# Kernel optimization log

Hardware: AMD Instinct MI355X
Metric: run time of the kernel (lower is better)

## Reference

```python
import jax, jax.numpy as jnp
import numpy as np

B, NC, H, W, C = 4, 3, 112, 112, 128
HEADS, WS, SS = 4, 7, 3
HD = C // HEADS
SCALE = HD ** -0.5
NWIN = (H // WS) * (W // WS)
N = WS * WS  # tokens per window per contrast


def _rel_pos_index():
    # standard Swin relative position index over a WSxWS window
    c = np.stack(np.meshgrid(np.arange(WS), np.arange(WS), indexing='ij')).reshape(2, -1)
    r = (c[:, :, None] - c[:, None, :]).transpose(1, 2, 0)
    r[:, :, 0] += WS - 1
    r[:, :, 1] += WS - 1
    r[:, :, 0] *= 2 * WS - 1
    return r.sum(-1)  # (N, N) int

RPI = _rel_pos_index()


def _attn_mask():
    # SW-MSA mask built exactly as in __init__ (shift active since 0 < SS < WS)
    img = np.zeros((H, W))
    sl = (slice(0, -WS), slice(-WS, -SS), slice(-SS, None))
    cnt = 0
    for hh in sl:
        for ww in sl:
            img[hh, ww] = cnt
            cnt += 1
    mw = img.reshape(H // WS, WS, W // WS, WS).transpose(0, 2, 1, 3).reshape(-1, N)
    am = mw[:, None, :] - mw[:, :, None]  # unsqueeze(1) - unsqueeze(2)
    return jnp.asarray(np.where(am != 0, -100.0, 0.0), dtype=np.float32)  # (nW, N, N)

MASK = _attn_mask()


def win_part(x):
    # (B, n, H, W, C) -> (B*nW, n, WS, WS, C)
    b, n = x.shape[0], x.shape[1]
    x = x.reshape(b, n, H // WS, WS, W // WS, WS, C)
    return x.transpose(0, 2, 4, 1, 3, 5, 6).reshape(-1, n, WS, WS, C)


def win_rev(x, b):
    # (B*nW, n, WS, WS, C) -> (B, n, H, W, C)
    n = x.shape[1]
    x = x.reshape(b, H // WS, W // WS, n, WS, WS, C)
    return x.transpose(0, 3, 1, 4, 2, 5, 6).reshape(b, n, H, W, C)


def ln(x, g, bta):
    m = x.mean(-1, keepdims=True)
    v = ((x - m) ** 2).mean(-1, keepdims=True)
    return (x - m) * jax.lax.rsqrt(v + 1e-5) * g + bta


def win_attn(xq, xk, xv, wq, bq, wk, bk, wv, bv, wp, bp, rpb):
    B_, nq = xq.shape[0], xq.shape[1]
    nkv = xk.shape[1]
    Nq, Nkv = nq * N, nkv * N
    q = (xq.reshape(B_, Nq, C) @ wq + bq).reshape(B_, Nq, HEADS, HD).transpose(0, 2, 1, 3) * SCALE
    k = (xk.reshape(B_, Nkv, C) @ wk + bk).reshape(B_, Nkv, HEADS, HD).transpose(0, 2, 1, 3)
    v = (xv.reshape(B_, Nkv, C) @ wv + bv).reshape(B_, Nkv, HEADS, HD).transpose(0, 2, 1, 3)
    attn = jnp.einsum('bhqd,bhkd->bhqk', q, k)
    bias = jnp.tile(rpb[RPI].transpose(2, 0, 1), (1, nq, nkv))  # (HEADS, Nq, Nkv)
    attn = attn + bias[None]
    m = jnp.tile(MASK, (1, nq, nkv))  # (nW, Nq, Nkv)
    attn = attn.reshape(B_ // NWIN, NWIN, HEADS, Nq, Nkv) + m[None, :, None]
    attn = jax.nn.softmax(attn.reshape(B_, HEADS, Nq, Nkv), axis=-1)
    out = jnp.einsum('bhqk,bhkd->bhqd', attn, v).transpose(0, 2, 1, 3).reshape(B_, Nq, C) @ wp + bp
    return out.reshape(B_, nq, WS, WS, C)


def reference(x, x_kv, contrast_token, contrast_embed,
              n1g, n1b, n2g, n2b, n3g, n3b,
              sa_wq, sa_bq, sa_wk, sa_bk, sa_wv, sa_bv, sa_wp, sa_bp, sa_rpb,
              ca_wq, ca_bq, ca_wk, ca_bk, ca_wv, ca_bv, ca_wp, ca_bp, ca_rpb,
              m_w1, m_b1, m_w2, m_b2):
    ct = contrast_token[None, :, None, None, :]
    ce = contrast_embed[None, :, None, None, :]
    # --- shifted-window self-attention ---
    shortcut = x
    h = ln(x, n1g, n1b)
    h = jnp.roll(h, (-SS, -SS), axis=(2, 3))
    xw = win_part(h)
    xwe = xw + ct
    aw = win_attn(xwe, xwe, xw, sa_wq, sa_bq, sa_wk, sa_bk, sa_wv, sa_bv, sa_wp, sa_bp, sa_rpb)
    h = win_rev(aw, B)
    h = jnp.roll(h, (SS, SS), axis=(2, 3))
    x = shortcut + h
    # --- shifted-window cross-attention against x_kv ---
    shortcut = x
    h = ln(x, n2g, n2b)
    hs = jnp.roll(h, (-SS, -SS), axis=(2, 3))
    kvs = jnp.roll(x_kv, (-SS, -SS), axis=(2, 3))
    xw = win_part(hs)
    kw = win_part(kvs)
    aw = win_attn(xw + ct, kw + ce, kw, ca_wq, ca_bq, ca_wk, ca_bk, ca_wv, ca_bv, ca_wp, ca_bp, ca_rpb)
    h = win_rev(aw, B)
    h = jnp.roll(h, (SS, SS), axis=(2, 3))
    x = shortcut + h
    # --- MLP ---
    h = ln(x, n3g, n3b)
    h = jax.nn.gelu(h @ m_w1 + m_b1, approximate=False) @ m_w2 + m_b2
    return x + h


def setup_inputs():
    key = jax.random.key(0)
    ks = jax.random.split(key, 32)
    rn = lambda i, shp, s=1.0: jax.random.normal(ks[i], shp, dtype=jnp.float32) * s
    inp = {
        'x': rn(0, (B, NC, H, W, C)),
        'x_kv': rn(1, (B, NC, H, W, C)),
        'contrast_token': rn(2, (NC, C), 0.02),
        'contrast_embed': rn(3, (NC, C), 0.02),
        'n1g': jnp.ones((C,)), 'n1b': jnp.zeros((C,)),
        'n2g': jnp.ones((C,)), 'n2b': jnp.zeros((C,)),
        'n3g': jnp.ones((C,)), 'n3b': jnp.zeros((C,)),
    }
    i = 4
    for pre in ('sa', 'ca'):
        for nm in ('wq', 'wk', 'wv', 'wp'):
            inp[pre + '_' + nm] = rn(i, (C, C), 0.02)
            inp[pre + '_b' + nm[1]] = jnp.zeros((C,))
            i += 1
        inp[pre + '_rpb'] = rn(i, ((2 * WS - 1) ** 2, HEADS), 0.02)
        i += 1
    inp['m_w1'] = rn(i, (C, 4 * C), 0.02)
    inp['m_b1'] = jnp.zeros((4 * C,))
    inp['m_w2'] = rn(i + 1, (4 * C, C), 0.02)
    inp['m_b2'] = jnp.zeros((C,))
    return inp
```

## Files before the change

kernel.cpp:

```cpp
#include <hip/hip_runtime.h>
#include <hip/hip_bf16.h>

typedef __hip_bfloat16 bf16;

#define Bn    4
#define NCn   3
#define Hn    112
#define Wn    112
#define Cn    128
#define HEADS 4
#define WSn   7
#define SSn   3
#define HDn   32
#define WNt   1024
#define Tt    147
#define SCALE 0.17677669529663687f

#define SA    288
#define SH    1056
#define MT    48
#define MTOK  80

static const size_t NE = (size_t)Bn * NCn * Hn * Wn * Cn;

typedef float f32x4 __attribute__((ext_vector_type(4)));
typedef short s16x8 __attribute__((ext_vector_type(8)));
typedef short s16x4 __attribute__((ext_vector_type(4)));
#define MFMA(a,b,c) __builtin_amdgcn_mfma_f32_16x16x32_bf16((a),(b),(c),0,0,0)

#define P_QCSA 0
#define P_KCSA 384
#define P_QCCA 768
#define P_KCCA 1152
#define P_VCSA 1536
#define P_BPSA 1664
#define P_VCCA 1792
#define P_BPCA 1920
#define P_B1   2048
#define P_B2   2560
#define P_G1   2688
#define P_N1B  2816
#define P_G2   2944
#define P_N2B  3072
#define P_G3   3200
#define P_N3B  3328
#define P_RPBSA 3456
#define P_RPBCA 4132

#define W_SAQ 0
#define W_SAK 16384
#define W_SAV 32768
#define W_SAP 49152
#define W_CAQ 65536
#define W_CAK 81920
#define W_CAV 98304
#define W_CAP 114688
#define W_W1T 131072
#define W_W2T 196608

struct Ptrs { const void* p[32]; };

__device__ __forceinline__ float bf2f(bf16 v) { return __bfloat162float(v); }
__device__ __forceinline__ bf16  f2bf(float v) { return __float2bfloat16(v); }
__device__ __forceinline__ short f2bs(float v) { bf16 t = __float2bfloat16(v); return *reinterpret_cast<short*>(&t); }
__device__ __forceinline__ float bs2f(short v) { bf16 t = *reinterpret_cast<bf16*>(&v); return __bfloat162float(t); }

__device__ __forceinline__ float ldi(const void* __restrict__ p, size_t i, int f) {
    return f ? ((const float*)p)[i] : bf2f(((const bf16*)p)[i]);
}

__device__ __forceinline__ float gelu(float x) {
    float x2 = x * x;
    float arg = x * fmaf(x2, 0.0713548162f, 1.5957691216f);
    float e = __expf(arg);
    float r = __builtin_amdgcn_rcpf(1.f + e);
    return x - x * r;
}

__device__ __forceinline__ int tok_row(int wn, int t) {
    int b = wn >> 8, wrem = wn & 255, wi = wrem >> 4, wj = wrem & 15;
    int n = t / 49, p = t % 49, pi = p / 7, pj = p % 7;
    int i = (wi * 7 + pi + SSn) % Hn;
    int j = (wj * 7 + pj + SSn) % Wn;
    return ((b * NCn + n) * Hn + i) * Wn + j;
}

__global__ void k_detect(const unsigned int* __restrict__ xw, int* __restrict__ flag) {
    __shared__ int cnt;
    if (threadIdx.x == 0) cnt = 0;
    __syncthreads();
    int c = 0;
    for (int i = threadIdx.x; i < 8192; i += 256) {
        unsigned e = (xw[i] >> 7) & 0xffu;
        c += (e >= 100u && e <= 140u) ? 1 : 0;
    }
    atomicAdd(&cnt, c);
    __syncthreads();
    if (threadIdx.x == 0) *flag = (cnt < 4096) ? 1 : 0;
}

__global__ __launch_bounds__(256) void k_prep(Ptrs in, const int* __restrict__ dflag,
                                              float* __restrict__ P, bf16* __restrict__ wT,
                                              float* __restrict__ BMT) {
    const int f = *dflag;
    int b = blockIdx.x, tid = threadIdx.x;
    if (b == 0) {
        for (int t = tid; t < 384; t += 256) {
            int n = t >> 7, c = t & 127;
            float aq = 0.f, ak = 0.f, aq2 = 0.f, ak2 = 0.f;
            for (int d = 0; d < Cn; ++d) {
                float ctv = ldi(in.p[2], n * Cn + d, f);
                float cev = ldi(in.p[3], n * Cn + d, f);
                aq  += ctv * ldi(in.p[10], d * Cn + c, f);
                ak  += ctv * ldi(in.p[12], d * Cn + c, f);
                aq2 += ctv * ldi(in.p[19], d * Cn + c, f);
                ak2 += cev * ldi(in.p[21], d * Cn + c, f);
            }
            P[P_QCSA + t] = aq  + ldi(in.p[11], c, f);
            P[P_KCSA + t] = ak  + ldi(in.p[13], c, f);
            P[P_QCCA + t] = aq2 + ldi(in.p[20], c, f);
            P[P_KCCA + t] = ak2 + ldi(in.p[22], c, f);
        }
    } else if (b == 1) {
        if (tid < 128) {
            P[P_VCSA + tid] = ldi(in.p[15], tid, f);
            P[P_BPSA + tid] = ldi(in.p[17], tid, f);
            P[P_VCCA + tid] = ldi(in.p[24], tid, f);
            P[P_BPCA + tid] = ldi(in.p[26], tid, f);
            P[P_B2   + tid] = ldi(in.p[31], tid, f);
            P[P_G1   + tid] = ldi(in.p[4],  tid, f);
            P[P_N1B  + tid] = ldi(in.p[5],  tid, f);
            P[P_G2   + tid] = ldi(in.p[6],  tid, f);
            P[P_N2B  + tid] = ldi(in.p[7],  tid, f);
            P[P_G3   + tid] = ldi(in.p[8],  tid, f);
            P[P_N3B  + tid] = ldi(in.p[9],  tid, f);
        }
        for (int t = tid; t < 512; t += 256) P[P_B1 + t] = ldi(in.p[29], t, f);
    } else if (b < 66) {
        const int map[8] = {10, 12, 14, 16, 19, 21, 23, 25};
        int unit = (b - 2) * 4 + (tid >> 6), lane = tid & 63;
        int mat = unit >> 5, ntks = unit & 31;
        int ntile = ntks >> 2, ks = ntks & 3;
        int n = ntile * 16 + (lane & 15), k0 = ks * 32 + (lane >> 4) * 8;
        const void* src = in.p[map[mat]];
        s16x8 v;
        #pragma unroll
        for (int j = 0; j < 8; ++j) v[j] = f2bs(ldi(src, (size_t)(k0 + j) * 128 + n, f));
        *(s16x8*)(wT + mat * 16384 + ((size_t)ntks * 64 + lane) * 8) = v;
    } else if (b < 130) {
        int unit = (b - 66) * 4 + (tid >> 6), lane = tid & 63;
        s16x8 v;
        if (unit < 128) {
            int ntile = unit >> 2, ks = unit & 3;
            int n = ntile * 16 + (lane & 15), k0 = ks * 32 + (lane >> 4) * 8;
            #pragma unroll
            for (int j = 0; j < 8; ++j) v[j] = f2bs(ldi(in.p[28], (size_t)(k0 + j) * 512 + n, f));
            *(s16x8*)(wT + W_W1T + ((size_t)unit * 64 + lane) * 8) = v;
        } else {
            int b2 = unit - 128;
            int ntile = b2 >> 4, ks = b2 & 15;
            int n = ntile * 16 + (lane & 15), k0 = ks * 32 + (lane >> 4) * 8;
            #pragma unroll
            for (int j = 0; j < 8; ++j) v[j] = f2bs(ldi(in.p[30], (size_t)(k0 + j) * 128 + n, f));
            *(s16x8*)(wT + W_W2T + ((size_t)b2 * 64 + lane) * 8) = v;
        }
    } else {
        int u = b - 130;
        int stage = u >> 4, pat = (u >> 2) & 3, h = u & 3;
        const void* rpb = in.p[stage ? 27 : 18];
        float* dst = BMT + (size_t)u * 2560;
        int er = pat >> 1, ec = pat & 1;
        for (int i = tid; i < 2560; i += 256) {
            float v = 0.f;
            int qp = i / 52, kp = i - qp * 52;
            if (qp < 49 && kp < 49) {
                int qpi = qp / 7, qpj = qp - qpi * 7, kpi = kp / 7, kpj = kp - kpi * 7;
                float bias = ldi(rpb, ((qpi - kpi + 6) * 13 + (qpj - kpj + 6)) * HEADS + h, f);
                int rq = (er ? (qpi < 4 ? 1 : 2) : 0) * 3 + (ec ? (qpj < 4 ? 1 : 2) : 0);
                int rk = (er ? (kpi < 4 ? 1 : 2) : 0) * 3 + (ec ? (kpj < 4 ? 1 : 2) : 0);
                v = bias + (rq == rk ? 0.f : -100.f);
            }
            dst[i] = v;
        }
    }
}

__device__ __forceinline__ void ln_inplace(char* __restrict__ rp, const float* __restrict__ gb) {
    float s = 0.f, s2 = 0.f;
    #pragma unroll
    for (int c8 = 0; c8 < 16; ++c8) {
        s16x8 v = *(const s16x8*)(rp + c8 * 16);
        #pragma unroll
        for (int j = 0; j < 8; ++j) { float fv = bs2f(v[j]); s += fv; s2 += fv * fv; }
    }
    float mean = s * (1.f / 128.f);
    float rstd = rsqrtf(s2 * (1.f / 128.f) - mean * mean + 1e-5f);
    #pragma unroll
    for (int c8 = 0; c8 < 16; ++c8) {
        s16x8 v = *(const s16x8*)(rp + c8 * 16);
        #pragma unroll
        for (int j = 0; j < 8; ++j) {
            int col = c8 * 8 + j;
            v[j] = f2bs((bs2f(v[j]) - mean) * rstd * gb[col] + gb[128 + col]);
        }
        *(s16x8*)(rp + c8 * 16) = v;
    }
}

__global__ __launch_bounds__(256) void k_qkv_sa(
    const void* __restrict__ x, bf16* __restrict__ xr,
    const float* __restrict__ P, const bf16* __restrict__ wT,
    const int* __restrict__ dflag,
    bf16* __restrict__ tokQ, bf16* __restrict__ tokK, bf16* __restrict__ tokV) {
    const int f = *dflag;
    __shared__ char ldsA[MTOK * SA];
    __shared__ int rowIdx[MTOK];
    __shared__ float gb[256];
    int wn = blockIdx.x, halfb = blockIdx.y, tid = threadIdx.x;
    int t0 = halfb * MTOK;
    int nrows = halfb ? (Tt - MTOK) : MTOK;
    if (tid < nrows) rowIdx[tid] = tok_row(wn, t0 + tid);
    gb[tid] = tid < 128 ? P[P_G1 + tid] : P[P_N1B + tid - 128];
    if (halfb) for (int i = tid; i < 13 * SA / 4; i += 256) ((int*)(ldsA + 67 * SA))[i] = 0;
    __syncthreads();
    for (int idx = tid; idx < nrows * 16; idx += 256) {
        int t = idx >> 4, c8 = idx & 15;
        size_t g = (size_t)rowIdx[t] * Cn + c8 * 8;
        s16x8 v;
        if (f) {
            const float* s = (const float*)x + g;
            #pragma unroll
            for (int j = 0; j < 8; ++j) v[j] = f2bs(s[j]);
        } else {
            v = *(const s16x8*)((const bf16*)x + g);
        }
        *(s16x8*)(ldsA + t * SA + c8 * 16) = v;
        *(s16x8*)(xr + g) = v;
    }
    __syncthreads();
    if (tid < nrows) ln_inplace(ldsA + tid * SA, gb);
    __syncthreads();
    int wv = tid >> 6, lane = tid & 63, l15 = lane & 15, lg = lane >> 4;
    #pragma unroll 1
    for (int mat = 0; mat < 3; ++mat) {
        const bf16* W = wT + mat * 16384;
        bf16* dst = mat == 0 ? tokQ : (mat == 1 ? tokK : tokV);
        #pragma unroll 1
        for (int ni = 0; ni < 2; ++ni) {
            int nt = wv * 2 + ni;
            f32x4 acc[5] = {};
            #pragma unroll
            for (int ks = 0; ks < 4; ++ks) {
                s16x8 bfrag = *(const s16x8*)(W + (((nt << 2) + ks) * 64 + lane) * 8);
                #pragma unroll
                for (int mt = 0; mt < 5; ++mt) {
                    s16x8 af = *(const s16x8*)(ldsA + (mt * 16 + l15) * SA + ks * 64 + lg * 16);
                    acc[mt] = MFMA(bfrag, af, acc[mt]);
                }
            }
            int col0 = nt * 16 + lg * 4;
            #pragma unroll
            for (int mt = 0; mt < 5; ++mt) {
                int tl = mt * 16 + l15;
                if (tl < nrows) {
                    int t = t0 + tl;
                    int n = t / 49;
                    s16x4 pk;
                    if (mat == 0) {
                        f32x4 b4 = *(const f32x4*)(P + P_QCSA + n * 128 + col0);
                        #pragma unroll
                        for (int r = 0; r < 4; ++r) pk[r] = f2bs((acc[mt][r] + b4[r]) * SCALE);
                    } else if (mat == 1) {
                        f32x4 b4 = *(const f32x4*)(P + P_KCSA + n * 128 + col0);
                        #pragma unroll
                        for (int r = 0; r < 4; ++r) pk[r] = f2bs(acc[mt][r] + b4[r]);
                    } else {
                        f32x4 b4 = *(const f32x4*)(P + P_VCSA + col0);
                        #pragma unroll
                        for (int r = 0; r < 4; ++r) pk[r] = f2bs(acc[mt][r] + b4[r]);
                    }
                    *(s16x4*)(dst + ((size_t)wn * Tt + t) * Cn + col0) = pk;
                }
            }
        }
    }
}

__global__ __launch_bounds__(256) void k_attn(
    const bf16* __restrict__ Q, const bf16* __restrict__ K, const bf16* __restrict__ V,
    bf16* __restrict__ O, const float* __restrict__ BMbase) {
    __shared__ char ldsK[40 * 256];
    __shared__ char ldsV[32 * 336];
    __shared__ char ldsP[4 * 16 * 336];
    __shared__ float BM[2560];
    __shared__ float lArr[4][16];
    int wn = blockIdx.x, h = blockIdx.y, tid = threadIdx.x;
    int wi = (wn >> 4) & 15, wj = wn & 15;
    size_t base = (size_t)wn * Tt * Cn + h * HDn;
    for (int idx = tid; idx < 640; idx += 256) {
        int key = idx >> 2, ch = idx & 3;
        s16x8 kv = {}, vv = {};
        if (key < Tt) {
            kv = *(const s16x8*)(K + base + (size_t)key * Cn + ch * 8);
            vv = *(const s16x8*)(V + base + (size_t)key * Cn + ch * 8);
        }
        *(s16x8*)(ldsK + (key >> 2) * 256 + (key & 3) * 64 + ch * 16) = kv;
        #pragma unroll
        for (int j = 0; j < 8; ++j)
            *(short*)(ldsV + (ch * 8 + j) * 336 + key * 2) = vv[j];
    }
    {
        int pat = ((wi == 15) << 1) | (wj == 15);
        const f32x4* src = (const f32x4*)(BMbase + (size_t)(pat * 4 + h) * 2560);
        f32x4* dst4 = (f32x4*)BM;
        for (int i = tid; i < 640; i += 256) dst4[i] = src[i];
    }
    __syncthreads();
    int wv = tid >> 6, lane = tid & 63, l15 = lane & 15, lg = lane >> 4;
    char* myP = ldsP + wv * (16 * 336);
    int kpA[10];
    #pragma unroll
    for (int nt = 0; nt < 10; ++nt) {
        int key = nt * 16 + l15;
        kpA[nt] = key - (key >= 147 ? 147 : (key >= 98 ? 98 : (key >= 49 ? 49 : 0)));
    }
    for (int mt = wv; mt < 10; mt += 4) {
        int qrow = mt * 16 + l15; if (qrow > 146) qrow = 146;
        s16x8 qf = *(const s16x8*)(Q + base + (size_t)qrow * Cn + lg * 8);
        f32x4 acc[10];
        #pragma unroll
        for (int nt = 0; nt < 10; ++nt) {
            int key = nt * 16 + l15;
            s16x8 bfrag = *(const s16x8*)(ldsK + (key >> 2) * 256 + (key & 3) * 64 + lg * 16);
            f32x4 z = {};
            acc[nt] = MFMA(qf, bfrag, z);
        }
        float linv[4];
        #pragma unroll
        for (int r = 0; r < 4; ++r) {
            int row = mt * 16 + lg * 4 + r;
            int qp = row - (row >= 147 ? 147 : (row >= 98 ? 98 : (row >= 49 ? 49 : 0)));
            float s[10], m = -1e30f;
            #pragma unroll
            for (int nt = 0; nt < 10; ++nt) {
                float sv = acc[nt][r] + BM[qp * 52 + kpA[nt]];
                if (nt == 9 && l15 >= 3) sv = -1e30f;
                s[nt] = sv;
                m = fmaxf(m, sv);
            }
            #pragma unroll
            for (int off = 1; off < 16; off <<= 1) m = fmaxf(m, __shfl_xor(m, off));
            float l = 0.f;
            #pragma unroll
            for (int nt = 0; nt < 10; ++nt) {
                float p = (nt == 9 && l15 >= 3) ? 0.f : __expf(s[nt] - m);
                l += p;
                *(bf16*)(myP + (lg * 4 + r) * 336 + (nt * 16 + l15) * 2) = f2bf(p);
            }
            #pragma unroll
            for (int off = 1; off < 16; off <<= 1) l += __shfl_xor(l, off);
            linv[r] = 1.f / l;
        }
        if (l15 == 0) {
            #pragma unroll
            for (int r = 0; r < 4; ++r) lArr[wv][lg * 4 + r] = linv[r];
        }
        float myinv = lArr[wv][l15];
        #pragma unroll
        for (int ntv = 0; ntv < 2; ++ntv) {
            f32x4 ao = {};
            #pragma unroll
            for (int ks = 0; ks < 5; ++ks) {
                s16x8 af = *(const s16x8*)(myP + l15 * 336 + ks * 64 + lg * 16);
                s16x8 vf = *(const s16x8*)(ldsV + (ntv * 16 + l15) * 336 + ks * 64 + lg * 16);
                ao = MFMA(vf, af, ao);
            }
            int q = mt * 16 + l15;
            if (q < Tt) {
                s16x4 pk;
                #pragma unroll
                for (int r = 0; r < 4; ++r) pk[r] = f2bs(ao[r] * myinv);
                *(s16x4*)(O + base + (size_t)q * Cn + ntv * 16 + lg * 4) = pk;
            }
        }
    }
}

__global__ __launch_bounds__(256) void k_proj(
    const bf16* __restrict__ tokO, const float* __restrict__ P, const bf16* __restrict__ W,
    int bpOff, bf16* __restrict__ xr) {
    __shared__ char ldsA[MTOK * SA];
    __shared__ int rowIdx[MTOK];
    int wn = blockIdx.x, halfb = blockIdx.y, tid = threadIdx.x;
    int t0 = halfb * MTOK;
    int nrows = halfb ? (Tt - MTOK) : MTOK;
    if (tid < nrows) rowIdx[tid] = tok_row(wn, t0 + tid);
    if (halfb) for (int i = tid; i < 13 * SA / 4; i += 256) ((int*)(ldsA + 67 * SA))[i] = 0;
    __syncthreads();
    for (int idx = tid; idx < nrows * 16; idx += 256) {
        int t = idx >> 4, c8 = idx & 15;
        s16x8 v = *(const s16x8*)(tokO + ((size_t)wn * Tt + t0 + t) * Cn + c8 * 8);
        *(s16x8*)(ldsA + t * SA + c8 * 16) = v;
    }
    __syncthreads();
    int wv = tid >> 6, lane = tid & 63, l15 = lane & 15, lg = lane >> 4;
    #pragma unroll 1
    for (int ni = 0; ni < 2; ++ni) {
        int nt = wv * 2 + ni;
        f32x4 acc[5] = {};
        #pragma unroll
        for (int ks = 0; ks < 4; ++ks) {
            s16x8 bfrag = *(const s16x8*)(W + (((nt << 2) + ks) * 64 + lane) * 8);
            #pragma unroll
            for (int mt = 0; mt < 5; ++mt) {
                s16x8 af = *(const s16x8*)(ldsA + (mt * 16 + l15) * SA + ks * 64 + lg * 16);
                acc[mt] = MFMA(bfrag, af, acc[mt]);
            }
        }
        int col0 = nt * 16 + lg * 4;
        f32x4 bp4 = *(const f32x4*)(P + bpOff + col0);
        #pragma unroll
        for (int mt = 0; mt < 5; ++mt) {
            int tl = mt * 16 + l15;
            if (tl < nrows) {
                size_t o = (size_t)rowIdx[tl] * Cn + col0;
                s16x4 cur = *(const s16x4*)(xr + o);
                s16x4 pk;
                #pragma unroll
                for (int r = 0; r < 4; ++r) pk[r] = f2bs(bs2f(cur[r]) + acc[mt][r] + bp4[r]);
                *(s16x4*)(xr + o) = pk;
            }
        }
    }
}

__global__ __launch_bounds__(256) void k_proj_ca(
    const bf16* __restrict__ tokO, const float* __restrict__ P, const bf16* __restrict__ wT,
    const void* __restrict__ xkv, const int* __restrict__ dflag, bf16* __restrict__ xr,
    bf16* __restrict__ tokQ, bf16* __restrict__ tokK, bf16* __restrict__ tokV) {
    const int f = *dflag;
    __shared__ char ldsA[MTOK * SA];
    __shared__ int rowIdx[MTOK];
    __shared__ float gb[256];
    int wn = blockIdx.x, halfb = blockIdx.y, tid = threadIdx.x;
    int t0 = halfb * MTOK;
    int nrows = halfb ? (Tt - MTOK) : MTOK;
    if (tid < nrows) rowIdx[tid] = tok_row(wn, t0 + tid);
    gb[tid] = tid < 128 ? P[P_G2 + tid] : P[P_N2B + tid - 128];
    if (halfb) for (int i = tid; i < 13 * SA / 4; i += 256) ((int*)(ldsA + 67 * SA))[i] = 0;
    __syncthreads();
    for (int idx = tid; idx < nrows * 16; idx += 256) {
        int t = idx >> 4, c8 = idx & 15;
        s16x8 v = *(const s16x8*)(tokO + ((size_t)wn * Tt + t0 + t) * Cn + c8 * 8);
        *(s16x8*)(ldsA + t * SA + c8 * 16) = v;
    }
    __syncthreads();
    int wv = tid >> 6, lane = tid & 63, l15 = lane & 15, lg = lane >> 4;
    {
        const bf16* W = wT + W_SAP;
        #pragma unroll 1
        for (int ni = 0; ni < 2; ++ni) {
            int nt = wv * 2 + ni;
            f32x4 acc[5] = {};
            #pragma unroll
            for (int ks = 0; ks < 4; ++ks) {
                s16x8 bfrag = *(const s16x8*)(W + (((nt << 2) + ks) * 64 + lane) * 8);
                #pragma unroll
                for (int mt = 0; mt < 5; ++mt) {
                    s16x8 af = *(const s16x8*)(ldsA + (mt * 16 + l15) * SA + ks * 64 + lg * 16);
                    acc[mt] = MFMA(bfrag, af, acc[mt]);
                }
            }
            int col0 = nt * 16 + lg * 4;
            f32x4 bp4 = *(const f32x4*)(P + P_BPSA + col0);
            #pragma unroll
            for (int mt = 0; mt < 5; ++mt) {
                int tl = mt * 16 + l15;
                if (tl < nrows) {
                    size_t o = (size_t)rowIdx[tl] * Cn + col0;
                    s16x4 cur = *(const s16x4*)(xr + o);
                    s16x4 pk;
                    #pragma unroll
                    for (int r = 0; r < 4; ++r) pk[r] = f2bs(bs2f(cur[r]) + acc[mt][r] + bp4[r]);
                    *(s16x4*)(xr + o) = pk;
                }
            }
        }
    }
    __syncthreads();
    for (int idx = tid; idx < nrows * 16; idx += 256) {
        int t = idx >> 4, c8 = idx & 15;
        s16x8 v = *(const s16x8*)(xr + (size_t)rowIdx[t] * Cn + c8 * 8);
        *(s16x8*)(ldsA + t * SA + c8 * 16) = v;
    }
    __syncthreads();
    if (tid < nrows) ln_inplace(ldsA + tid * SA, gb);
    __syncthreads();
    {
        const bf16* W = wT + W_CAQ;
        #pragma unroll 1
        for (int ni = 0; ni < 2; ++ni) {
            int nt = wv * 2 + ni;
            f32x4 acc[5] = {};
            #pragma unroll
            for (int ks = 0; ks < 4; ++ks) {
                s16x8 bfrag = *(const s16x8*)(W + (((nt << 2) + ks) * 64 + lane) * 8);
                #pragma unroll
                for (int mt = 0; mt < 5; ++mt) {
                    s16x8 af = *(const s16x8*)(ldsA + (mt * 16 + l15) * SA + ks * 64 + lg * 16);
                    acc[mt] = MFMA(bfrag, af, acc[mt]);
                }
            }
            int col0 = nt * 16 + lg * 4;
            #pragma unroll
            for (int mt = 0; mt < 5; ++mt) {
                int tl = mt * 16 + l15;
                if (tl < nrows) {
                    int t = t0 + tl;
                    int n = t / 49;
                    f32x4 b4 = *(const f32x4*)(P + P_QCCA + n * 128 + col0);
                    s16x4 pk;
                    #pragma unroll
                    for (int r = 0; r < 4; ++r) pk[r] = f2bs((acc[mt][r] + b4[r]) * SCALE);
                    *(s16x4*)(tokQ + ((size_t)wn * Tt + t) * Cn + col0) = pk;
                }
            }
        }
    }
    __syncthreads();
    for (int idx = tid; idx < nrows * 16; idx += 256) {
        int t = idx >> 4, c8 = idx & 15;
        s16x8 v;
        if (f) {
            const float* s = (const float*)xkv + (size_t)rowIdx[t] * Cn + c8 * 8;
            #pragma unroll
            for (int j = 0; j < 8; ++j) v[j] = f2bs(s[j]);
        } else {
            v = *(const s16x8*)((const bf16*)xkv + (size_t)rowIdx[t] * Cn + c8 * 8);
        }
        *(s16x8*)(ldsA + t * SA + c8 * 16) = v;
    }
    __syncthreads();
    #pragma unroll 1
    for (int mat = 0; mat < 2; ++mat) {
        const bf16* W = wT + (mat == 0 ? W_CAK : W_CAV);
        bf16* dst = mat == 0 ? tokK : tokV;
        #pragma unroll 1
        for (int ni = 0; ni < 2; ++ni) {
            int nt = wv * 2 + ni;
            f32x4 acc[5] = {};
            #pragma unroll
            for (int ks = 0; ks < 4; ++ks) {
                s16x8 bfrag = *(const s16x8*)(W + (((nt << 2) + ks) * 64 + lane) * 8);
                #pragma unroll
                for (int mt = 0; mt < 5; ++mt) {
                    s16x8 af = *(const s16x8*)(ldsA + (mt * 16 + l15) * SA + ks * 64 + lg * 16);
                    acc[mt] = MFMA(bfrag, af, acc[mt]);
                }
            }
            int col0 = nt * 16 + lg * 4;
            #pragma unroll
            for (int mt = 0; mt < 5; ++mt) {
                int tl = mt * 16 + l15;
                if (tl < nrows) {
                    int t = t0 + tl;
                    int n = t / 49;
                    f32x4 b4 = (mat == 0) ? *(const f32x4*)(P + P_KCCA + n * 128 + col0)
                                          : *(const f32x4*)(P + P_VCCA + col0);
                    s16x4 pk;
                    #pragma unroll
                    for (int r = 0; r < 4; ++r) pk[r] = f2bs(acc[mt][r] + b4[r]);
                    *(s16x4*)(dst + ((size_t)wn * Tt + t) * Cn + col0) = pk;
                }
            }
        }
    }
}

__global__ __launch_bounds__(256) void k_mlp(
    const bf16* __restrict__ xr, const float* __restrict__ P, const bf16* __restrict__ wT,
    const int* __restrict__ dflag, void* __restrict__ outp) {
    __shared__ char ldsU[MT * SH];
    __shared__ float gb[256];
    char* ldsA = ldsU;
    char* ldsH = ldsU;
    int tid = threadIdx.x;
    size_t t0 = (size_t)blockIdx.x * MT;
    gb[tid] = tid < 128 ? P[P_G3 + tid] : P[P_N3B + tid - 128];
    __syncthreads();
    for (int idx = tid; idx < MT * 16; idx += 256) {
        int t = idx >> 4, c8 = idx & 15;
        s16x8 v = *(const s16x8*)(xr + (t0 + t) * Cn + c8 * 8);
        *(s16x8*)(ldsA + t * SA + c8 * 16) = v;
    }
    __syncthreads();
    {
        int row = tid >> 2, sub = tid & 3;
        if (row < MT) {
            char* rp = ldsA + row * SA + sub * 64;
            float s = 0.f, s2 = 0.f;
            s16x8 vv[4];
            #pragma unroll
            for (int c = 0; c < 4; ++c) {
                vv[c] = *(const s16x8*)(rp + c * 16);
                #pragma unroll
                for (int j = 0; j < 8; ++j) { float fv = bs2f(vv[c][j]); s += fv; s2 += fv * fv; }
            }
            s  += __shfl_xor(s, 1);  s  += __shfl_xor(s, 2);
            s2 += __shfl_xor(s2, 1); s2 += __shfl_xor(s2, 2);
            float mean = s * (1.f / 128.f);
            float rstd = rsqrtf(s2 * (1.f / 128.f) - mean * mean + 1e-5f);
            #pragma unroll
            for (int c = 0; c < 4; ++c) {
                #pragma unroll
                for (int j = 0; j < 8; ++j) {
                    int col = sub * 32 + c * 8 + j;
                    vv[c][j] = f2bs((bs2f(vv[c][j]) - mean) * rstd * gb[col] + gb[128 + col]);
                }
                *(s16x8*)(rp + c * 16) = vv[c];
            }
        }
    }
    __syncthreads();
    int wv = tid >> 6, lane = tid & 63, l15 = lane & 15, lg = lane >> 4;
    const bf16* W1 = wT + W_W1T;
    s16x8 a[3][4];
    #pragma unroll
    for (int m = 0; m < 3; ++m)
        #pragma unroll
        for (int ks = 0; ks < 4; ++ks)
            a[m][ks] = *(const s16x8*)(ldsA + (m * 16 + l15) * SA + ks * 64 + lg * 16);
    __syncthreads();
    {
        int nt0 = wv * 8;
        s16x8 bc0 = *(const s16x8*)(W1 + (((nt0 << 2) + 0) * 64 + lane) * 8);
        s16x8 bc1 = *(const s16x8*)(W1 + (((nt0 << 2) + 1) * 64 + lane) * 8);
        s16x8 bc2 = *(const s16x8*)(W1 + (((nt0 << 2) + 2) * 64 + lane) * 8);
        s16x8 bc3 = *(const s16x8*)(W1 + (((nt0 << 2) + 3) * 64 + lane) * 8);
        #pragma unroll 1
        for (int ni = 0; ni < 8; ++ni) {
            int nt = nt0 + ni;
            s16x8 bn0 = *(const s16x8*)(W1 + ((((nt + 1) << 2) + 0) * 64 + lane) * 8);
            s16x8 bn1 = *(const s16x8*)(W1 + ((((nt + 1) << 2) + 1) * 64 + lane) * 8);
            s16x8 bn2 = *(const s16x8*)(W1 + ((((nt + 1) << 2) + 2) * 64 + lane) * 8);
            s16x8 bn3 = *(const s16x8*)(W1 + ((((nt + 1) << 2) + 3) * 64 + lane) * 8);
            f32x4 acc[3] = {};
            #pragma unroll
            for (int m = 0; m < 3; ++m) {
                acc[m] = MFMA(bc0, a[m][0], acc[m]);
                acc[m] = MFMA(bc1, a[m][1], acc[m]);
                acc[m] = MFMA(bc2, a[m][2], acc[m]);
                acc[m] = MFMA(bc3, a[m][3], acc[m]);
            }
            int col0 = nt * 16 + lg * 4;
            f32x4 b14 = *(const f32x4*)(P + P_B1 + col0);
            #pragma unroll
            for (int m = 0; m < 3; ++m) {
                s16x4 pk;
                #pragma unroll
                for (int r = 0; r < 4; ++r) pk[r] = f2bs(gelu(acc[m][r] + b14[r]));
                *(s16x4*)(ldsH + (m * 16 + l15) * SH + col0 * 2) = pk;
            }
            bc0 = bn0; bc1 = bn1; bc2 = bn2; bc3 = bn3;
        }
    }
    __syncthreads();
    const int f = *dflag;
    const bf16* W2 = wT + W_W2T;
    #pragma unroll 1
    for (int ni = 0; ni < 2; ++ni) {
        int nt = wv * 2 + ni;
        f32x4 acc[3] = {};
        s16x8 bc = *(const s16x8*)(W2 + (((nt << 4) + 0) * 64 + lane) * 8);
        #pragma unroll 1
        for (int ks = 0; ks < 16; ++ks) {
            s16x8 bn = *(const s16x8*)(W2 + (((nt << 4) + ks + 1) * 64 + lane) * 8);
            #pragma unroll
            for (int m = 0; m < 3; ++m) {
                s16x8 af = *(const s16x8*)(ldsH + (m * 16 + l15) * SH + ks * 64 + lg * 16);
                acc[m] = MFMA(bc, af, acc[m]);
            }
            bc = bn;
        }
        int col0 = nt * 16 + lg * 4;
        f32x4 b24 = *(const f32x4*)(P + P_B2 + col0);
        #pragma unroll
        for (int m = 0; m < 3; ++m) {
            size_t g = (t0 + m * 16 + l15) * Cn + col0;
            s16x4 cur = *(const s16x4*)(xr + g);
            if (f) {
                f32x4 o;
                #pragma unroll
                for (int r = 0; r < 4; ++r) o[r] = bs2f(cur[r]) + acc[m][r] + b24[r];
                *(f32x4*)((float*)outp + g) = o;
            } else {
                s16x4 pk;
                #pragma unroll
                for (int r = 0; r < 4; ++r) pk[r] = f2bs(bs2f(cur[r]) + acc[m][r] + b24[r]);
                *(s16x4*)((bf16*)outp + g) = pk;
            }
        }
    }
}

extern "C" void kernel_launch(void* const* d_in, const int* in_sizes, int n_in,
                              void* d_out, int out_size, void* d_ws, size_t ws_size,
                              hipStream_t stream) {
    Ptrs ptrs;
    for (int i = 0; i < 32; ++i) ptrs.p[i] = d_in[i];

    char* base = (char*)d_ws;
    float* P    = (float*)base;
    int*  dflag = (int*)(base + 32768);
    bf16* wT    = (bf16*)(base + 33024);
    float* BMT  = (float*)(wT + 262144);
    bf16* xr    = (bf16*)(BMT + 81920);
    bf16* tokK  = xr + NE;
    bf16* tokV  = tokK + NE;
    bf16* tokQ  = (bf16*)d_out;

    k_detect<<<1, 256, 0, stream>>>((const unsigned int*)d_in[0], dflag);
    k_prep<<<162, 256, 0, stream>>>(ptrs, dflag, P, wT, BMT);
    k_qkv_sa<<<dim3(WNt, 2), 256, 0, stream>>>(d_in[0], xr, P, wT, dflag, tokQ, tokK, tokV);
    k_attn<<<dim3(WNt, HEADS), 256, 0, stream>>>(tokQ, tokK, tokV, tokQ, BMT);
    k_proj_ca<<<dim3(WNt, 2), 256, 0, stream>>>(tokQ, P, wT, d_in[1], dflag, xr, tokQ, tokK, tokV);
    k_attn<<<dim3(WNt, HEADS), 256, 0, stream>>>(tokQ, tokK, tokV, tokQ, BMT + 16 * 2560);
    k_proj<<<dim3(WNt, 2), 256, 0, stream>>>(tokQ, P, wT + W_CAP, P_BPCA, xr);
    k_mlp<<<(int)(NE / Cn / MT), 256, 0, stream>>>(xr, P, wT, dflag, d_out);
}
```

Measured before the change: 593.0 us.

## Prefetch residual and KV tiles early; write projected residual directly into LDS

In the projection kernels, the residual values of xr are loaded into registers before the GEMM instead of after it, and both N-tiles are accumulated together. The epilogue then no longer waits on a dependent global read. In k_proj_ca, the x_kv tile is staged into a second LDS buffer at kernel start. The post-projection residual is also written straight into LDS, which removes a global reload and two barriers. The cost is higher register pressure (20 accumulators plus cached residuals) and doubled LDS use per block, which may lower occupancy.

```diff
diff --git a/kernel.cpp b/kernel.cpp
--- a/kernel.cpp
+++ b/kernel.cpp
@@ -44,8 +44,6 @@
 #define P_N2B  3072
 #define P_G3   3200
 #define P_N3B  3328
-#define P_RPBSA 3456
-#define P_RPBCA 4132
 
 #define W_SAQ 0
 #define W_SAK 16384
@@ -397,38 +395,50 @@
     if (tid < nrows) rowIdx[tid] = tok_row(wn, t0 + tid);
     if (halfb) for (int i = tid; i < 13 * SA / 4; i += 256) ((int*)(ldsA + 67 * SA))[i] = 0;
     __syncthreads();
+    int wv = tid >> 6, lane = tid & 63, l15 = lane & 15, lg = lane >> 4;
+    s16x4 xrc[2][5];
+    #pragma unroll
+    for (int ni = 0; ni < 2; ++ni) {
+        int col0 = (wv * 2 + ni) * 16 + lg * 4;
+        #pragma unroll
+        for (int mt = 0; mt < 5; ++mt) {
+            int tl = mt * 16 + l15;
+            int rr = rowIdx[tl < nrows ? tl : 0];
+            xrc[ni][mt] = *(const s16x4*)(xr + (size_t)rr * Cn + col0);
+        }
+    }
     for (int idx = tid; idx < nrows * 16; idx += 256) {
         int t = idx >> 4, c8 = idx & 15;
         s16x8 v = *(const s16x8*)(tokO + ((size_t)wn * Tt + t0 + t) * Cn + c8 * 8);
         *(s16x8*)(ldsA + t * SA + c8 * 16) = v;
     }
     __syncthreads();
-    int wv = tid >> 6, lane = tid & 63, l15 = lane & 15, lg = lane >> 4;
-    #pragma unroll 1
+    f32x4 acc2[2][5] = {};
+    #pragma unroll
     for (int ni = 0; ni < 2; ++ni) {
         int nt = wv * 2 + ni;
-        f32x4 acc[5] = {};
         #pragma unroll
         for (int ks = 0; ks < 4; ++ks) {
             s16x8 bfrag = *(const s16x8*)(W + (((nt << 2) + ks) * 64 + lane) * 8);
             #pragma unroll
             for (int mt = 0; mt < 5; ++mt) {
                 s16x8 af = *(const s16x8*)(ldsA + (mt * 16 + l15) * SA + ks * 64 + lg * 16);
-                acc[mt] = MFMA(bfrag, af, acc[mt]);
-            }
-        }
-        int col0 = nt * 16 + lg * 4;
+                acc2[ni][mt] = MFMA(bfrag, af, acc2[ni][mt]);
+            }
+        }
+    }
+    #pragma unroll
+    for (int ni = 0; ni < 2; ++ni) {
+        int col0 = (wv * 2 + ni) * 16 + lg * 4;
         f32x4 bp4 = *(const f32x4*)(P + bpOff + col0);
         #pragma unroll
         for (int mt = 0; mt < 5; ++mt) {
             int tl = mt * 16 + l15;
             if (tl < nrows) {
-                size_t o = (size_t)rowIdx[tl] * Cn + col0;
-                s16x4 cur = *(const s16x4*)(xr + o);
                 s16x4 pk;
                 #pragma unroll
-                for (int r = 0; r < 4; ++r) pk[r] = f2bs(bs2f(cur[r]) + acc[mt][r] + bp4[r]);
-                *(s16x4*)(xr + o) = pk;
+                for (int r = 0; r < 4; ++r) pk[r] = f2bs(bs2f(xrc[ni][mt][r]) + acc2[ni][mt][r] + bp4[r]);
+                *(s16x4*)(xr + (size_t)rowIdx[tl] * Cn + col0) = pk;
             }
         }
     }
@@ -440,6 +450,7 @@
     bf16* __restrict__ tokQ, bf16* __restrict__ tokK, bf16* __restrict__ tokV) {
     const int f = *dflag;
     __shared__ char ldsA[MTOK * SA];
+    __shared__ char ldsB[MTOK * SA];
     __shared__ int rowIdx[MTOK];
     __shared__ float gb[256];
     int wn = blockIdx.x, halfb = blockIdx.y, tid = threadIdx.x;
@@ -447,8 +458,25 @@
     int nrows = halfb ? (Tt - MTOK) : MTOK;
     if (tid < nrows) rowIdx[tid] = tok_row(wn, t0 + tid);
     gb[tid] = tid < 128 ? P[P_G2 + tid] : P[P_N2B + tid - 128];
-    if (halfb) for (int i = tid; i < 13 * SA / 4; i += 256) ((int*)(ldsA + 67 * SA))[i] = 0;
-    __syncthreads();
+    if (halfb) {
+        for (int i = tid; i < 13 * SA / 4; i += 256) {
+            ((int*)(ldsA + 67 * SA))[i] = 0;
+            ((int*)(ldsB + 67 * SA))[i] = 0;
+        }
+    }
+    __syncthreads();
+    for (int idx = tid; idx < nrows * 16; idx += 256) {
+        int t = idx >> 4, c8 = idx & 15;
+        s16x8 v;
+        if (f) {
+            const float* s = (const float*)xkv + (size_t)rowIdx[t] * Cn + c8 * 8;
+            #pragma unroll
+            for (int j = 0; j < 8; ++j) v[j] = f2bs(s[j]);
+        } else {
+            v = *(const s16x8*)((const bf16*)xkv + (size_t)rowIdx[t] * Cn + c8 * 8);
+        }
+        *(s16x8*)(ldsB + t * SA + c8 * 16) = v;
+    }
     for (int idx = tid; idx < nrows * 16; idx += 256) {
         int t = idx >> 4, c8 = idx & 15;
         s16x8 v = *(const s16x8*)(tokO + ((size_t)wn * Tt + t0 + t) * Cn + c8 * 8);
@@ -456,42 +484,50 @@
     }
     __syncthreads();
     int wv = tid >> 6, lane = tid & 63, l15 = lane & 15, lg = lane >> 4;
+    s16x4 xrc[2][5];
+    #pragma unroll
+    for (int ni = 0; ni < 2; ++ni) {
+        int col0 = (wv * 2 + ni) * 16 + lg * 4;
+        #pragma unroll
+        for (int mt = 0; mt < 5; ++mt) {
+            int tl = mt * 16 + l15;
+            int rr = rowIdx[tl < nrows ? tl : 0];
+            xrc[ni][mt] = *(const s16x4*)(xr + (size_t)rr * Cn + col0);
+        }
+    }
+    f32x4 acc2[2][5] = {};
     {
         const bf16* W = wT + W_SAP;
-        #pragma unroll 1
+        #pragma unroll
         for (int ni = 0; ni < 2; ++ni) {
             int nt = wv * 2 + ni;
-            f32x4 acc[5] = {};
             #pragma unroll
             for (int ks = 0; ks < 4; ++ks) {
                 s16x8 bfrag = *(const s16x8*)(W + (((nt << 2) + ks) * 64 + lane) * 8);
                 #pragma unroll
                 for (int mt = 0; mt < 5; ++mt) {
                     s16x8 af = *(const s16x8*)(ldsA + (mt * 16 + l15) * SA + ks * 64 + lg * 16);
-                    acc[mt] = MFMA(bfrag, af, acc[mt]);
+                    acc2[ni][mt] = MFMA(bfrag, af, acc2[ni][mt]);
                 }
             }
-            int col0 = nt * 16 + lg * 4;
-            f32x4 bp4 = *(const f32x4*)(P + P_BPSA + col0);
-            #pragma unroll
-            for (int mt = 0; mt < 5; ++mt) {
-                int tl = mt * 16 + l15;
-                if (tl < nrows) {
-                    size_t o = (size_t)rowIdx[tl] * Cn + col0;
-                    s16x4 cur = *(const s16x4*)(xr + o);
-                    s16x4 pk;
-                    #pragma unroll
-                    for (int r = 0; r < 4; ++r) pk[r] = f2bs(bs2f(cur[r]) + acc[mt][r] + bp4[r]);
-                    *(s16x4*)(xr + o) = pk;
-                }
-            }
-        }
-    }
-    __syncthreads();
-    for (int idx = tid; idx < nrows * 16; idx += 256) {
-        int t = idx >> 4, c8 = idx & 15;
-        s16x8 v = *(const s16x8*)(xr + (size_t)rowIdx[t] * Cn + c8 * 8);
-        *(s16x8*)(ldsA + t * SA + c8 * 16) = v;
+        }
+    }
+    __syncthreads();
+    #pragma unroll
+    for (int ni = 0; ni < 2; ++ni) {
+        int col0 = (wv * 2 + ni) * 16 + lg * 4;
+        f32x4 bp4 = *(const f32x4*)(P + P_BPSA + col0);
+        #pragma unroll
+        for (int mt = 0; mt < 5; ++mt) {
+            int tl = mt * 16 + l15;
+            if (tl < nrows) {
+                s16x4 pk;
+                #pragma unroll
+                for (int r = 0; r < 4; ++r) pk[r] = f2bs(bs2f(xrc[ni][mt][r]) + acc2[ni][mt][r] + bp4[r]);
+                *(s16x4*)(xr + (size_t)rowIdx[tl] * Cn + col0) = pk;
+                *(s16x4*)(ldsA + tl * SA + col0 * 2) = pk;
+            }
+        }
     }
     __syncthreads();
     if (tid < nrows) ln_inplace(ldsA + tid * SA, gb);
@@ -527,20 +563,6 @@
             }
         }
     }
-    __syncthreads();
-    for (int idx = tid; idx < nrows * 16; idx += 256) {
-        int t = idx >> 4, c8 = idx & 15;
-        s16x8 v;
-        if (f) {
-            const float* s = (const float*)xkv + (size_t)rowIdx[t] * Cn + c8 * 8;
-            #pragma unroll
-            for (int j = 0; j < 8; ++j) v[j] = f2bs(s[j]);
-        } else {
-            v = *(const s16x8*)((const bf16*)xkv + (size_t)rowIdx[t] * Cn + c8 * 8);
-        }
-        *(s16x8*)(ldsA + t * SA + c8 * 16) = v;
-    }
-    __syncthreads();
     #pragma unroll 1
     for (int mat = 0; mat < 2; ++mat) {
         const bf16* W = wT + (mat == 0 ? W_CAK : W_CAV);
@@ -554,7 +576,7 @@
                 s16x8 bfrag = *(const s16x8*)(W + (((nt << 2) + ks) * 64 + lane) * 8);
                 #pragma unroll
                 for (int mt = 0; mt < 5; ++mt) {
-                    s16x8 af = *(const s16x8*)(ldsA + (mt * 16 + l15) * SA + ks * 64 + lg * 16);
+                    s16x8 af = *(const s16x8*)(ldsB + (mt * 16 + l15) * SA + ks * 64 + lg * 16);
                     acc[mt] = MFMA(bfrag, af, acc[mt]);
                 }
             }
```

New measurement: 601.4 us. About the same (+1.4%).
